# Kernel optimization log

Hardware: AMD Instinct MI355X
Metric: run time of the kernel (lower is better)

## Reference

```python
import jax, jax.numpy as jnp
import numpy as np

B, S, D, H = 2, 2048, 1024, 16
DH = D // H  # 64


def setup_inputs() -> dict:
    key = jax.random.key(0)
    k1, k2, k3, k4 = jax.random.split(key, 4)
    x = jax.random.normal(k1, (B, S, D), dtype=jnp.float32)
    # causal mask: 0 => masked (matches mask==0 -> -inf in source)
    mask = jnp.tril(jnp.ones((S, S), dtype=jnp.int32))
    Wq = jax.random.normal(k2, (H, D, DH), dtype=jnp.float32) * (D ** -0.5)
    Wk = jax.random.normal(k3, (H, D, DH), dtype=jnp.float32) * (D ** -0.5)
    Wo = jax.random.normal(k4, (D, D), dtype=jnp.float32) * (D ** -0.5)
    bo = jnp.zeros((D,), dtype=jnp.float32)
    return {"x": x, "mask": mask, "Wq": Wq, "Wk": Wk, "Wo": Wo, "bo": bo}


def reference(x, mask, Wq, Wk, Wo, bo):
    # Per source: q = query(x), k = key(x), v = query(x)  (bug kept: v == q)
    q = jnp.einsum('bsd,hde->bhse', x, Wq)   # [B,H,S,DH]
    k = jnp.einsum('bsd,hde->bhse', x, Wk)   # [B,H,S,DH]
    # scale uses d_model (input dim), not d_head -- faithful to source
    scale = jnp.asarray(D, x.dtype) ** -0.5
    scores = jnp.einsum('bhse,bhte->bhst', q, k) * scale  # [B,H,S,S]
    neg_inf = jnp.asarray(float('-inf'), scores.dtype)
    scores = jnp.where(mask[None, None, :, :] == 0, neg_inf, scores)
    w = jax.nn.softmax(scores, axis=-1)
    attn = jnp.einsum('bhst,bhte->bhse', w, q)  # v == q
    # concat heads: head axis becomes contiguous feature blocks
    attn = attn.transpose(0, 2, 1, 3).reshape(B, S, D)
    return attn @ Wo + bo
```

## Files before the change

kernel.cpp:

```cpp
#include <hip/hip_runtime.h>
#include <hip/hip_bf16.h>

#define BQ 2
#define SQ 2048
#define DMODEL 1024
#define NH 16
#define DH 64
#define NQT (SQ / 64)

typedef __attribute__((ext_vector_type(8))) short bf16x8;
typedef __attribute__((ext_vector_type(4))) float f32x4;
typedef unsigned short u16;

__device__ __forceinline__ u16 f2b(float f) {
  __hip_bfloat16 h = __float2bfloat16(f);
  return *reinterpret_cast<u16*>(&h);
}

#define MFMA(a, b, c) __builtin_amdgcn_mfma_f32_16x16x32_bf16((a), (b), (c), 0, 0, 0)

#define CS (0.03125f * 1.44269504088896f)


__global__ void cvt_x_kernel(const float* __restrict__ x, u16* __restrict__ xb, int n) {
  int i = blockIdx.x * blockDim.x + threadIdx.x;
  int stride = gridDim.x * blockDim.x;
  for (; i < n; i += stride) xb[i] = f2b(x[i]);
}

__global__ void transpose_head_kernel(const float* __restrict__ W, u16* __restrict__ WT) {
  int i = blockIdx.x * blockDim.x + threadIdx.x;
  const int total = NH * DMODEL * DH;
  int stride = gridDim.x * blockDim.x;
  for (; i < total; i += stride) {
    int h = i >> 16;
    int rem = i & 65535;
    int e = rem >> 10;
    int d = rem & 1023;
    WT[i] = f2b(W[((size_t)(h << 10) + d) * DH + e]);
  }
}

__global__ void transpose_wo_kernel(const float* __restrict__ Wo, u16* __restrict__ WoT) {
  int i = blockIdx.x * blockDim.x + threadIdx.x;
  const int total = DMODEL * DMODEL;
  int stride = gridDim.x * blockDim.x;
  for (; i < total; i += stride) {
    int nn = i >> 10, kk = i & 1023;
    WoT[i] = f2b(Wo[(size_t)kk * DMODEL + nn]);
  }
}

__global__ __launch_bounds__(256) void transpose_q_kernel(
    const u16* __restrict__ Q, u16* __restrict__ QT) {
  __shared__ alignas(16) u16 T[64][72];
  int st = blockIdx.x, h = blockIdx.y, b = blockIdx.z;
  size_t hb = ((size_t)(b * NH + h)) * SQ * DH;
  int tid = threadIdx.x;
#pragma unroll
  for (int i2 = 0; i2 < 2; ++i2) {
    int c = tid + i2 * 256;
    int r = c >> 3, cc = (c & 7) * 8;
    *(uint4*)&T[r][cc] = *(const uint4*)&Q[hb + (size_t)(st * 64 + r) * DH + cc];
  }
  __syncthreads();
#pragma unroll
  for (int i2 = 0; i2 < 2; ++i2) {
    int c = tid + i2 * 256;
    int e = c >> 3, s8 = (c & 7) * 8;
    u16 tmp[8];
#pragma unroll
    for (int j = 0; j < 8; ++j) tmp[j] = T[s8 + j][e];
    *(uint4*)&QT[hb + (size_t)e * SQ + st * 64 + s8] = *(uint4*)tmp;
  }
}


__global__ __launch_bounds__(256) void proj_kernel(
    const u16* __restrict__ xb,
    const u16* __restrict__ Wcat,
    u16* __restrict__ Qb, u16* __restrict__ Kb) {
  __shared__ alignas(16) u16 Xs[64][72];
  __shared__ alignas(16) u16 Ws[64][72];
  int st = blockIdx.x, hy = blockIdx.y, b = blockIdx.z;
  int tid = threadIdx.x;
  int w = tid >> 6, l = tid & 63;
  int lr = l & 15, lk = (l >> 4) * 8;
  f32x4 acc[4] = {};
  const u16* Ab = xb + (size_t)(b * SQ + st * 64) * DMODEL;
  const u16* Wb = Wcat + (size_t)hy * DH * DMODEL;
  for (int k0 = 0; k0 < DMODEL; k0 += 64) {
#pragma unroll
    for (int i2 = 0; i2 < 2; ++i2) {
      int c = tid + i2 * 256;
      int r = c >> 3, cc = (c & 7) * 8;
      *(uint4*)&Xs[r][cc] = *(const uint4*)&Ab[(size_t)r * DMODEL + k0 + cc];
      *(uint4*)&Ws[r][cc] = *(const uint4*)&Wb[(size_t)r * DMODEL + k0 + cc];
    }
    __syncthreads();
#pragma unroll
    for (int kk = 0; kk < 2; ++kk) {
      bf16x8 a = *(const bf16x8*)&Xs[w * 16 + lr][kk * 32 + lk];
#pragma unroll
      for (int n = 0; n < 4; ++n) {
        bf16x8 bb = *(const bf16x8*)&Ws[n * 16 + lr][kk * 32 + lk];
        acc[n] = MFMA(a, bb, acc[n]);
      }
    }
    __syncthreads();
  }
  bool isQ = (hy < NH);
  u16* dst = isQ ? Qb : Kb;
  float scale = isQ ? 1.0f : CS;
  int hh = hy & (NH - 1);
  size_t obase = ((size_t)(b * NH + hh) * SQ + st * 64) * DH;
  int r0 = w * 16 + ((l >> 4) << 2);
#pragma unroll
  for (int n = 0; n < 4; ++n)
#pragma unroll
    for (int r = 0; r < 4; ++r)
      dst[obase + (size_t)(r0 + r) * DH + n * 16 + lr] = f2b(acc[n][r] * scale);
}


__global__ __launch_bounds__(512) void attn_kernel(
    const u16* __restrict__ Qt,
    const u16* __restrict__ Kt,
    const u16* __restrict__ QTt,
    u16* __restrict__ Oc) {
  __shared__ alignas(16) u16 Ks[2][64][72];
  __shared__ alignas(16) u16 Vs[2][64][72];
  __shared__ alignas(16) u16 Ps[8][16][80];
  int bx = blockIdx.x, h = blockIdx.y, b = blockIdx.z;
  int p = b ? bx : (15 - bx);
  int tid = threadIdx.x, w = tid >> 6, l = tid & 63;
  int lr = l & 15, lk = (l >> 4) * 8, hi = l >> 4;
  int qtile = 2 * p + (w >> 2);
  int q0 = qtile * 64 + (w & 3) * 16;
  int jmax = 2 * p + 1;
  size_t hb = ((size_t)(b * NH + h)) * SQ * DH;

  int r0s = tid >> 3, cc0 = (tid & 7) * 8;

  bf16x8 aq[2];
  {
    const u16* qrow = Qt + hb + (size_t)(q0 + lr) * DH;
    aq[0] = *(const bf16x8*)&qrow[lk];
    aq[1] = *(const bf16x8*)&qrow[32 + lk];
  }

  *(uint4*)&Ks[0][r0s][cc0] = *(const uint4*)&Kt[hb + (size_t)r0s * DH + cc0];
  *(uint4*)&Vs[0][r0s][cc0] = *(const uint4*)&QTt[hb + (size_t)r0s * SQ + cc0];
  __syncthreads();

  uint4 kreg = *(const uint4*)&Kt[hb + (size_t)(64 + r0s) * DH + cc0];
  uint4 vreg = *(const uint4*)&QTt[hb + (size_t)r0s * SQ + 64 + cc0];

  f32x4 acc[4] = {};
  float l_run[4] = {0.f, 0.f, 0.f, 0.f};
  int cur = 0;

  for (int j = 0; j <= jmax; ++j) {
    if (j <= qtile) {
      f32x4 s[4] = {};
#pragma unroll
      for (int kk = 0; kk < 2; ++kk)
#pragma unroll
        for (int n = 0; n < 4; ++n) {
          bf16x8 bk = *(const bf16x8*)&Ks[cur][n * 16 + lr][kk * 32 + lk];
          s[n] = MFMA(aq[kk], bk, s[n]);
        }

      if (j == qtile) {
        int rowg = q0 + (hi << 2);
#pragma unroll
        for (int n = 0; n < 4; ++n) {
          int kc = j * 64 + n * 16 + lr;
#pragma unroll
          for (int r = 0; r < 4; ++r)
            s[n][r] = (kc > rowg + r) ? 0.f : exp2f(s[n][r]);
        }
      } else {
#pragma unroll
        for (int n = 0; n < 4; ++n)
#pragma unroll
          for (int r = 0; r < 4; ++r) s[n][r] = exp2f(s[n][r]);
      }

#pragma unroll
      for (int r = 0; r < 4; ++r)
        l_run[r] += (s[0][r] + s[1][r]) + (s[2][r] + s[3][r]);

#pragma unroll
      for (int n = 0; n < 4; ++n)
#pragma unroll
        for (int r = 0; r < 4; ++r)
          Ps[w][(hi << 2) + r][n * 16 + lr] = f2b(s[n][r]);

#pragma unroll
      for (int kk = 0; kk < 2; ++kk) {
        bf16x8 ap = *(const bf16x8*)&Ps[w][lr][kk * 32 + lk];
#pragma unroll
        for (int n = 0; n < 4; ++n) {
          bf16x8 bv = *(const bf16x8*)&Vs[cur][n * 16 + lr][kk * 32 + lk];
          acc[n] = MFMA(ap, bv, acc[n]);
        }
      }
    }

    if (j < jmax) {
      *(uint4*)&Ks[cur ^ 1][r0s][cc0] = kreg;
      *(uint4*)&Vs[cur ^ 1][r0s][cc0] = vreg;
      if (j + 2 <= jmax) {
        kreg = *(const uint4*)&Kt[hb + (size_t)((j + 2) * 64 + r0s) * DH + cc0];
        vreg = *(const uint4*)&QTt[hb + (size_t)r0s * SQ + (j + 2) * 64 + cc0];
      }
      __syncthreads();
      cur ^= 1;
    }
  }

#pragma unroll
  for (int r = 0; r < 4; ++r) {
#pragma unroll
    for (int msk = 1; msk < 16; msk <<= 1)
      l_run[r] += __shfl_xor(l_run[r], msk, 64);
  }

#pragma unroll
  for (int r = 0; r < 4; ++r) {
    float inv = 1.f / l_run[r];
    size_t rbase = ((size_t)b * SQ + q0 + (hi << 2) + r) * DMODEL + h * DH;
#pragma unroll
    for (int n = 0; n < 4; ++n)
      Oc[rbase + n * 16 + lr] = f2b(acc[n][r] * inv);
  }
}


__global__ __launch_bounds__(256) void outproj_kernel(
    const u16* __restrict__ Oc,
    const u16* __restrict__ WoT,
    const float* __restrict__ bo,
    float* __restrict__ out) {
  __shared__ alignas(16) u16 Xs[64][72];
  __shared__ alignas(16) u16 Ws[64][72];
  int rt = blockIdx.x, nt = blockIdx.y;
  int tid = threadIdx.x, w = tid >> 6, l = tid & 63;
  int lr = l & 15, lk = (l >> 4) * 8;
  f32x4 acc[4] = {};
  const u16* Ab = Oc + (size_t)rt * 64 * DMODEL;
  const u16* Wb = WoT + (size_t)nt * 64 * DMODEL;
  for (int k0 = 0; k0 < DMODEL; k0 += 64) {
#pragma unroll
    for (int i2 = 0; i2 < 2; ++i2) {
      int c = tid + i2 * 256;
      int r = c >> 3, cc = (c & 7) * 8;
      *(uint4*)&Xs[r][cc] = *(const uint4*)&Ab[(size_t)r * DMODEL + k0 + cc];
      *(uint4*)&Ws[r][cc] = *(const uint4*)&Wb[(size_t)r * DMODEL + k0 + cc];
    }
    __syncthreads();
#pragma unroll
    for (int kk = 0; kk < 2; ++kk) {
      bf16x8 a = *(const bf16x8*)&Xs[w * 16 + lr][kk * 32 + lk];
#pragma unroll
      for (int n = 0; n < 4; ++n) {
        bf16x8 bb = *(const bf16x8*)&Ws[n * 16 + lr][kk * 32 + lk];
        acc[n] = MFMA(a, bb, acc[n]);
      }
    }
    __syncthreads();
  }
  int r0 = w * 16 + ((l >> 4) << 2);
#pragma unroll
  for (int n = 0; n < 4; ++n) {
    int col = nt * 64 + n * 16 + lr;
    float bv = bo[col];
#pragma unroll
    for (int r = 0; r < 4; ++r)
      out[(size_t)(rt * 64 + r0 + r) * DMODEL + col] = acc[n][r] + bv;
  }
}


extern "C" void kernel_launch(void* const* d_in, const int* in_sizes, int n_in,
                              void* d_out, int out_size, void* d_ws, size_t ws_size,
                              hipStream_t stream) {
  const float* x  = (const float*)d_in[0];
  const float* Wq = (const float*)d_in[2];
  const float* Wk = (const float*)d_in[3];
  const float* Wo = (const float*)d_in[4];
  const float* bo = (const float*)d_in[5];
  float* out = (float*)d_out;

  char* ws = (char*)d_ws;
  u16* xb  = (u16*)ws;
  u16* WqT = xb + (size_t)BQ * SQ * DMODEL;
  u16* WkT = WqT + (size_t)NH * DH * DMODEL;
  u16* WoT = WkT + (size_t)NH * DH * DMODEL;
  u16* Qb  = WoT + (size_t)DMODEL * DMODEL;
  u16* Kb  = Qb + (size_t)BQ * NH * SQ * DH;
  u16* Ob  = Kb + (size_t)BQ * NH * SQ * DH;
  u16* QTb = xb;

  cvt_x_kernel<<<2048, 256, 0, stream>>>(x, xb, BQ * SQ * DMODEL);
  transpose_head_kernel<<<2048, 256, 0, stream>>>(Wq, WqT);
  transpose_head_kernel<<<2048, 256, 0, stream>>>(Wk, WkT);
  transpose_wo_kernel<<<1024, 256, 0, stream>>>(Wo, WoT);

  proj_kernel<<<dim3(SQ / 64, 2 * NH, BQ), 256, 0, stream>>>(xb, WqT, Qb, Kb);
  transpose_q_kernel<<<dim3(SQ / 64, NH, BQ), 256, 0, stream>>>(Qb, QTb);
  attn_kernel<<<dim3(16, NH, BQ), 512, 0, stream>>>(Qb, Kb, QTb, Ob);
  outproj_kernel<<<dim3(BQ * SQ / 64, DMODEL / 64, 1), 256, 0, stream>>>(Ob, WoT, bo, out);
}
```

Before: 132.5 us.

## Compute transposed scores to keep P in registers, dropping LDS round-trip

Swaps the operands of the QK^T MFMA so each lane holds scores for a single query row along keys. The probabilities can then be packed to bf16 with v_cvt_pk_bf16_f32 and used directly as the B operand of 16x16x16 MFMAs, computing O^T with V rows loaded from LDS as the A operand. This removes the per-wave shared-memory P buffer, its writes and reads, and reduces the row-sum reduction to two cross-lane shuffles. In exchange it uses twice as many smaller MFMA instructions with narrower LDS loads for V, and writes output as packed 32-bit pairs.

```diff
diff --git a/kernel.cpp b/kernel.cpp
--- a/kernel.cpp
+++ b/kernel.cpp
@@ -9,6 +9,7 @@
 #define NQT (SQ / 64)
 
 typedef __attribute__((ext_vector_type(8))) short bf16x8;
+typedef __attribute__((ext_vector_type(4))) short bf16x4;
 typedef __attribute__((ext_vector_type(4))) float f32x4;
 typedef unsigned short u16;
 
@@ -18,6 +19,17 @@
 }
 
 #define MFMA(a, b, c) __builtin_amdgcn_mfma_f32_16x16x32_bf16((a), (b), (c), 0, 0, 0)
+
+__device__ __forceinline__ f32x4 mfma16(bf16x4 a, bf16x4 b, f32x4 c) {
+  asm("v_mfma_f32_16x16x16_bf16 %0, %1, %2, %0" : "+v"(c) : "v"(a), "v"(b));
+  return c;
+}
+
+__device__ __forceinline__ unsigned cvtpk(float lo, float hi) {
+  unsigned r;
+  asm("v_cvt_pk_bf16_f32 %0, %1, %2" : "=v"(r) : "v"(lo), "v"(hi));
+  return r;
+}
 
 #define CS (0.03125f * 1.44269504088896f)
 
@@ -130,11 +142,10 @@
     u16* __restrict__ Oc) {
   __shared__ alignas(16) u16 Ks[2][64][72];
   __shared__ alignas(16) u16 Vs[2][64][72];
-  __shared__ alignas(16) u16 Ps[8][16][80];
   int bx = blockIdx.x, h = blockIdx.y, b = blockIdx.z;
   int p = b ? bx : (15 - bx);
   int tid = threadIdx.x, w = tid >> 6, l = tid & 63;
-  int lr = l & 15, lk = (l >> 4) * 8, hi = l >> 4;
+  int lr = l & 15, hi = l >> 4, lk = hi * 8;
   int qtile = 2 * p + (w >> 2);
   int q0 = qtile * 64 + (w & 3) * 16;
   int jmax = 2 * p + 1;
@@ -156,8 +167,8 @@
   uint4 kreg = *(const uint4*)&Kt[hb + (size_t)(64 + r0s) * DH + cc0];
   uint4 vreg = *(const uint4*)&QTt[hb + (size_t)r0s * SQ + 64 + cc0];
 
-  f32x4 acc[4] = {};
-  float l_run[4] = {0.f, 0.f, 0.f, 0.f};
+  f32x4 acc_t[4] = {};
+  float l_run = 0.f;
   int cur = 0;
 
   for (int j = 0; j <= jmax; ++j) {
@@ -168,17 +179,17 @@
 #pragma unroll
         for (int n = 0; n < 4; ++n) {
           bf16x8 bk = *(const bf16x8*)&Ks[cur][n * 16 + lr][kk * 32 + lk];
-          s[n] = MFMA(aq[kk], bk, s[n]);
+          s[n] = MFMA(bk, aq[kk], s[n]);
         }
 
       if (j == qtile) {
-        int rowg = q0 + (hi << 2);
+        int qg = q0 + lr;
 #pragma unroll
         for (int n = 0; n < 4; ++n) {
-          int kc = j * 64 + n * 16 + lr;
+          int kbase = j * 64 + n * 16 + hi * 4;
 #pragma unroll
           for (int r = 0; r < 4; ++r)
-            s[n][r] = (kc > rowg + r) ? 0.f : exp2f(s[n][r]);
+            s[n][r] = (kbase + r > qg) ? 0.f : exp2f(s[n][r]);
         }
       } else {
 #pragma unroll
@@ -188,22 +199,25 @@
       }
 
 #pragma unroll
-      for (int r = 0; r < 4; ++r)
-        l_run[r] += (s[0][r] + s[1][r]) + (s[2][r] + s[3][r]);
-
-#pragma unroll
       for (int n = 0; n < 4; ++n)
-#pragma unroll
-        for (int r = 0; r < 4; ++r)
-          Ps[w][(hi << 2) + r][n * 16 + lr] = f2b(s[n][r]);
-
-#pragma unroll
-      for (int kk = 0; kk < 2; ++kk) {
-        bf16x8 ap = *(const bf16x8*)&Ps[w][lr][kk * 32 + lk];
-#pragma unroll
-        for (int n = 0; n < 4; ++n) {
-          bf16x8 bv = *(const bf16x8*)&Vs[cur][n * 16 + lr][kk * 32 + lk];
-          acc[n] = MFMA(ap, bv, acc[n]);
+        l_run += (s[n][0] + s[n][1]) + (s[n][2] + s[n][3]);
+
+      bf16x4 pb[4];
+#pragma unroll
+      for (int n = 0; n < 4; ++n) {
+        uint2 u;
+        u.x = cvtpk(s[n][0], s[n][1]);
+        u.y = cvtpk(s[n][2], s[n][3]);
+        pb[n] = *(bf16x4*)&u;
+      }
+
+#pragma unroll
+      for (int nv = 0; nv < 4; ++nv) {
+        const u16* vrow = &Vs[cur][nv * 16 + lr][hi * 4];
+#pragma unroll
+        for (int nh = 0; nh < 4; ++nh) {
+          bf16x4 va = *(const bf16x4*)&vrow[nh * 16];
+          acc_t[nv] = mfma16(va, pb[nh], acc_t[nv]);
         }
       }
     }
@@ -220,20 +234,18 @@
     }
   }
 
-#pragma unroll
-  for (int r = 0; r < 4; ++r) {
-#pragma unroll
-    for (int msk = 1; msk < 16; msk <<= 1)
-      l_run[r] += __shfl_xor(l_run[r], msk, 64);
-  }
-
-#pragma unroll
-  for (int r = 0; r < 4; ++r) {
-    float inv = 1.f / l_run[r];
-    size_t rbase = ((size_t)b * SQ + q0 + (hi << 2) + r) * DMODEL + h * DH;
-#pragma unroll
-    for (int n = 0; n < 4; ++n)
-      Oc[rbase + n * 16 + lr] = f2b(acc[n][r] * inv);
+  l_run += __shfl_xor(l_run, 16, 64);
+  l_run += __shfl_xor(l_run, 32, 64);
+  float inv = 1.f / l_run;
+
+  size_t rbase = ((size_t)b * SQ + q0 + lr) * DMODEL + h * DH;
+#pragma unroll
+  for (int nv = 0; nv < 4; ++nv) {
+#pragma unroll
+    for (int rp = 0; rp < 2; ++rp) {
+      unsigned pw = cvtpk(acc_t[nv][2 * rp] * inv, acc_t[nv][2 * rp + 1] * inv);
+      *(unsigned*)&Oc[rbase + nv * 16 + hi * 4 + 2 * rp] = pw;
+    }
   }
 }
 
```

New measurement: 130.0 us. About the same (-1.9%).
